# Performance work log

Hardware: AMD Instinct MI355X
Metric: run time of the kernel (lower is better)

## Reference

```python
import jax, jax.numpy as jnp
import numpy as np

NEG = -1e10  # matches the -10000000000.0 boundary padding in the torch code


def nw_forward(theta, A):
    """Needleman-Wunsch forward DP with softmax (logsumexp) operator.

    theta: (B, N, M) match potentials; A: (B,) gap penalty.
    Returns Vt: (B,) terminal alignment scores.
    Recursion: V[i,j] = theta[i-1,j-1] + logsumexp(A+V[i-1,j], V[i-1,j-1], A+V[i,j-1]).
    Implemented as scan over rows (i) with an inner scan over columns (j),
    which honors the sequential DP dependencies without Python loops.
    """
    B, N, M = theta.shape
    dtype = theta.dtype
    # V[0, :] row: V[0,0]=0, V[0,j]=NEG for j>=1
    row0 = jnp.full((B, M + 1), NEG, dtype).at[:, 0].set(0.0)

    def row_step(prev_row, th_row):
        # prev_row: (B, M+1) = V[i-1, 0..M]; th_row: (B, M) = theta[:, i-1, :]
        v_up = prev_row[:, 1:]     # V[i-1, j],   j = 1..M
        v_diag = prev_row[:, :-1]  # V[i-1, j-1], j = 1..M

        def col_step(v_left, inp):
            th_j, vu, vd = inp  # each (B,)
            # order (x, m, y) = (A+up, diag, A+left), matching torch stack(v1,v2,v3)
            v = jnp.stack([A + vu, vd, A + v_left], axis=-1)  # (B, 3)
            v_new = th_j + jax.nn.logsumexp(v, axis=-1)
            return v_new, v_new

        xs = (th_row.T, v_up.T, v_diag.T)  # leading axis M
        v_init = jnp.full((B,), NEG, dtype)  # V[i, 0]
        _, row_vals = jax.lax.scan(col_step, v_init, xs)  # (M, B)
        new_row = jnp.concatenate(
            [jnp.full((B, 1), NEG, dtype), row_vals.T], axis=1)  # (B, M+1)
        return new_row, None

    last_row, _ = jax.lax.scan(row_step, row0, jnp.moveaxis(theta, 1, 0))
    return last_row[:, M]  # Vt = V[:, N, M]


def setup_inputs() -> dict:
    key = jax.random.key(0)
    k1, k2 = jax.random.split(key)
    B, N, M = 32, 512, 512
    theta = jax.random.normal(k1, (B, N, M), dtype=jnp.float32)
    A = jax.random.normal(k2, (B,), dtype=jnp.float32)
    return {"theta": theta, "A": A}


def reference(theta, A):
    return nw_forward(theta, A)
```

## Files before the change

kernel.cpp:

```cpp
#include <hip/hip_runtime.h>
#include <math.h>

#define NEGV  -10000000000.0f
#define LOG2E 1.44269504088896340736f
#define LN2F  0.69314718055994530942f

typedef float f4 __attribute__((ext_vector_type(4)));

constexpr int CS    = 32;
constexpr int ROWS  = 96;
constexpr int WL    = 33;
constexpr int CHW   = ROWS * WL;
constexpr int KCMAX = 32;
constexpr int SIT   = 48;

__global__ __launch_bounds__(512, 2) void nw_kernel(
    const float* __restrict__ theta, const float* __restrict__ A,
    float* __restrict__ out, int N, int M)
{
    __shared__ float thS[8 * CHW];
    __shared__ float bndD[9 * KCMAX * CS];
    __shared__ int   flg[9 * KCMAX];

    const int tid = threadIdx.x;
    const int w   = tid >> 6;
    const int l   = tid & 63;
    const int j   = tid;
    const int b   = blockIdx.x;
    const int NW  = blockDim.x >> 6;

    for (int i = tid; i < 9 * KCMAX; i += blockDim.x) flg[i] = 0;
    __syncthreads();

    const float a2 = A[b] * LOG2E;
    const float* __restrict__ thb = theta + (size_t)b * N * M;
    const int NM = N * M;

    const int T  = N + M - 1;
    const int KC = (T + CS - 1) / CS;
    const int wstart = 64 * w;
    const int wend   = 64 * w + 63 + N - 1;
    const int ca = wstart / CS;
    const int cb = min(KC - 1, wend / CS);

    const int srow = l >> 5;
    const int sq   = l & 31;
    const int lanebase = srow * (M - 1) + 64 * w + 63 + sq;
    const int wrbase   = w * CHW + srow * WL + sq;
    const int rdbase   = w * CHW + (63 - l) * WL;

    auto stage_load = [&](int cn, float* stg) {
        const int rb = CS * cn - 64 * w - 63;
        if (rb >= 0 && rb + (ROWS - 1) <= N - 1) {
            const float* p = thb + (size_t)rb * M;
            #pragma unroll
            for (int it = 0; it < SIT; ++it) { stg[it] = p[lanebase]; p += 2 * (M - 1); }
        } else {
            const int rbM = rb * M;
            #pragma unroll
            for (int it = 0; it < SIT; ++it) {
                int off = rbM + lanebase + it * 2 * (M - 1);
                off = min(max(off, 0), NM - 1);
                stg[it] = thb[off];
            }
        }
    };
    auto stage_write = [&](const float* stg) {
        #pragma unroll
        for (int it = 0; it < SIT; ++it) thS[wrbase + it * 2 * WL] = stg[it] * LOG2E;
    };
    auto wait_flag = [&](int idx) {
        if (__atomic_load_n(&flg[idx], __ATOMIC_ACQUIRE) == 0) {
            do { __builtin_amdgcn_s_sleep(1); }
            while (__atomic_load_n(&flg[idx], __ATOMIC_ACQUIRE) == 0);
        }
    };

    float mp = NEGV, sp = 1.0f;
    float md = (j == 0) ? 0.0f : NEGV, sd = 1.0f;
    float bcarry = NEGV;

    {
        float s0[SIT];
        stage_load(ca, s0);
        stage_write(s0);
        __asm__ volatile("s_waitcnt lgkmcnt(0)" ::: "memory");
    }
    if (w > 0) {
        wait_flag(w * KCMAX + (ca - 1));
        bcarry = bndD[(w * KCMAX + ca - 1) * CS + (CS - 1)];
    }

    float stg[SIT];
    bool have = (ca + 1 <= cb);
    if (have) stage_load(ca + 1, stg);

    for (int c = ca; c <= cb; ++c) {
        float th[CS];
        #pragma unroll
        for (int k = 0; k < 8; ++k) th[k] = thS[rdbase + k * (WL + 1)];

        const bool need_bv = (w > 0) && (CS * c <= 64 * w + N - 1);
        float bv[CS];
        if (need_bv) {
            wait_flag(w * KCMAX + c);
            const f4* src = (const f4*)&bndD[(w * KCMAX + c) * CS];
            #pragma unroll
            for (int q = 0; q < CS / 4; ++q) {
                f4 t = src[q];
                bv[4*q+0] = t.x; bv[4*q+1] = t.y; bv[4*q+2] = t.z; bv[4*q+3] = t.w;
            }
        } else {
            #pragma unroll
            for (int k = 0; k < CS; ++k) bv[k] = NEGV;
        }

        #pragma unroll
        for (int k = 8; k < CS; ++k) th[k] = thS[rdbase + k * (WL + 1)];

        float res[CS];
        const bool full = (CS * c >= 64 * w + 63) &&
                          (CS * c + CS - 1 <= 64 * w + N - 1);
        if (full) {
            #pragma unroll
            for (int k = 0; k < CS; ++k) {
                float bm = (k == 0) ? bcarry : bv[k - 1];
                float ml = __int_as_float(__builtin_amdgcn_update_dpp(
                    __float_as_int(bm), __float_as_int(mp),
                    0x138 , 0xF, 0xF, false));
                float sl = __int_as_float(__builtin_amdgcn_update_dpp(
                    0x3f800000 , __float_as_int(sp),
                    0x138, 0xF, 0xF, false));
                float u  = a2 + mp;
                float ul = a2 + ml;
                float mx = fmaxf(fmaxf(u, md), ul);
                float e1 = __builtin_amdgcn_exp2f(u  - mx);
                float e2 = __builtin_amdgcn_exp2f(md - mx);
                float e3 = __builtin_amdgcn_exp2f(ul - mx);
                float sn = fmaf(sl, e3, fmaf(sd, e2, sp * e1));
                float mn = th[k] + mx;
                res[k] = mn + __builtin_amdgcn_logf(sn);
                md = ml; sd = sl;
                mp = mn; sp = sn;
            }
        } else {
            const int tmj = CS * c - j;
            #pragma unroll
            for (int k = 0; k < CS; ++k) {
                float bm = (k == 0) ? bcarry : bv[k - 1];
                float ml = __int_as_float(__builtin_amdgcn_update_dpp(
                    __float_as_int(bm), __float_as_int(mp),
                    0x138, 0xF, 0xF, false));
                float sl = __int_as_float(__builtin_amdgcn_update_dpp(
                    0x3f800000, __float_as_int(sp),
                    0x138, 0xF, 0xF, false));
                float u  = a2 + mp;
                float ul = a2 + ml;
                float mx = fmaxf(fmaxf(u, md), ul);
                float e1 = __builtin_amdgcn_exp2f(u  - mx);
                float e2 = __builtin_amdgcn_exp2f(md - mx);
                float e3 = __builtin_amdgcn_exp2f(ul - mx);
                float sn = fmaf(sl, e3, fmaf(sd, e2, sp * e1));
                float mn = th[k] + mx;
                int dt = tmj + k;
                bool act = (unsigned)dt < (unsigned)N;
                float mq = act ? mn : (dt < 0 ? NEGV : mp);
                float sq2 = act ? sn : (dt < 0 ? 1.0f : sp);
                res[k] = mq + __builtin_amdgcn_logf(sq2);
                md = ml; sd = sl;
                mp = mq; sp = sq2;
            }
        }

        if (w < NW - 1 && l == 63) {
            f4* dst = (f4*)&bndD[((w + 1) * KCMAX + c) * CS];
            #pragma unroll
            for (int q = 0; q < CS / 4; ++q)
                dst[q] = (f4){res[4*q+0], res[4*q+1], res[4*q+2], res[4*q+3]};
            __atomic_store_n(&flg[(w + 1) * KCMAX + c], 1, __ATOMIC_RELEASE);
        }
        bcarry = bv[CS - 1];

        {
            int bs = __float_as_int(sp);
            int ex = ((bs >> 23) & 0xff) - 127;
            sp = __int_as_float(bs - (ex << 23));
            mp += (float)ex;
            int bd = __float_as_int(sd);
            int ed = ((bd >> 23) & 0xff) - 127;
            sd = __int_as_float(bd - (ed << 23));
            md += (float)ed;
        }

        if (have) stage_write(stg);
        have = (c + 2 <= cb);
        if (have) stage_load(c + 2, stg);
        __asm__ volatile("s_waitcnt lgkmcnt(0)" ::: "memory");
    }

    if (j == M - 1)
        out[b] = (mp + __builtin_amdgcn_logf(sp)) * LN2F;
}

extern "C" void kernel_launch(void* const* d_in, const int* in_sizes, int n_in,
                              void* d_out, int out_size, void* d_ws, size_t ws_size,
                              hipStream_t stream) {
    const float* theta = (const float*)d_in[0];
    const float* A     = (const float*)d_in[1];
    float* out = (float*)d_out;

    const int B  = in_sizes[1];
    const int NM = in_sizes[0] / B;
    int N = 1;
    while (N * N < NM) N <<= 1;
    const int M = NM / N;

    hipLaunchKernelGGL(nw_kernel, dim3(B), dim3(M), 0, stream,
                       theta, A, out, N, M);
}
```

Before: 178.7 us.

## Stream theta tiles directly to LDS with global_load_lds and swizzled layout

Replaces the register-staged global load plus LDS write (48 registers per thread) with direct global-to-LDS loads. A XOR-style rotation swizzle replaces the padded row layout to avoid bank conflicts. The LOG2E scaling moves into an fma in the recurrence, and prefetch depth drops from two stages ahead to one stage issued during compute. This cuts register pressure and VALU/LDS-store work, but single-buffered LDS reuse requires waiting on lgkmcnt before issuing the next stage and vmcnt at loop end, which may expose load latency.

Result: slower. 256.6 us (+43.6%).

```diff
diff --git a/kernel.cpp b/kernel.cpp
--- a/kernel.cpp
+++ b/kernel.cpp
@@ -9,8 +9,7 @@
 
 constexpr int CS    = 32;
 constexpr int ROWS  = 96;
-constexpr int WL    = 33;
-constexpr int CHW   = ROWS * WL;
+constexpr int CHW   = ROWS * 32;
 constexpr int KCMAX = 32;
 constexpr int SIT   = 48;
 
@@ -43,31 +42,38 @@
     const int ca = wstart / CS;
     const int cb = min(KC - 1, wend / CS);
 
-    const int srow = l >> 5;
-    const int sq   = l & 31;
-    const int lanebase = srow * (M - 1) + 64 * w + 63 + sq;
-    const int wrbase   = w * CHW + srow * WL + sq;
-    const int rdbase   = w * CHW + (63 - l) * WL;
-
-    auto stage_load = [&](int cn, float* stg) {
+    const int l5  = l >> 5, l31 = l & 31;
+    const int q2  = l31 - l5;
+    const int q   = 63 - l;
+    float* thW = &thS[w * CHW];
+
+    auto issue_stage = [&](int cn) {
         const int rb = CS * cn - 64 * w - 63;
+        const int gbase = rb * M + 64 * w + 63;
         if (rb >= 0 && rb + (ROWS - 1) <= N - 1) {
-            const float* p = thb + (size_t)rb * M;
-            #pragma unroll
-            for (int it = 0; it < SIT; ++it) { stg[it] = p[lanebase]; p += 2 * (M - 1); }
+            #pragma unroll
+            for (int it = 0; it < SIT; ++it) {
+                const int r = 2 * it + l5;
+                const int c = (q2 - 2 * it) & 31;
+                const int gidx = gbase + r * (M - 1) + c;
+                __builtin_amdgcn_global_load_lds(
+                    (const __attribute__((address_space(1))) void*)(thb + gidx),
+                    (__attribute__((address_space(3))) void*)(thW + it * 64),
+                    4, 0, 0);
+            }
         } else {
-            const int rbM = rb * M;
             #pragma unroll
             for (int it = 0; it < SIT; ++it) {
-                int off = rbM + lanebase + it * 2 * (M - 1);
-                off = min(max(off, 0), NM - 1);
-                stg[it] = thb[off];
-            }
-        }
-    };
-    auto stage_write = [&](const float* stg) {
-        #pragma unroll
-        for (int it = 0; it < SIT; ++it) thS[wrbase + it * 2 * WL] = stg[it] * LOG2E;
+                const int r = 2 * it + l5;
+                const int c = (q2 - 2 * it) & 31;
+                int gidx = gbase + r * (M - 1) + c;
+                gidx = min(max(gidx, 0), NM - 1);
+                __builtin_amdgcn_global_load_lds(
+                    (const __attribute__((address_space(1))) void*)(thb + gidx),
+                    (__attribute__((address_space(3))) void*)(thW + it * 64),
+                    4, 0, 0);
+            }
+        }
     };
     auto wait_flag = [&](int idx) {
         if (__atomic_load_n(&flg[idx], __ATOMIC_ACQUIRE) == 0) {
@@ -80,25 +86,18 @@
     float md = (j == 0) ? 0.0f : NEGV, sd = 1.0f;
     float bcarry = NEGV;
 
-    {
-        float s0[SIT];
-        stage_load(ca, s0);
-        stage_write(s0);
-        __asm__ volatile("s_waitcnt lgkmcnt(0)" ::: "memory");
-    }
+    issue_stage(ca);
+    __asm__ volatile("s_waitcnt vmcnt(0)" ::: "memory");
     if (w > 0) {
         wait_flag(w * KCMAX + (ca - 1));
         bcarry = bndD[(w * KCMAX + ca - 1) * CS + (CS - 1)];
     }
 
-    float stg[SIT];
-    bool have = (ca + 1 <= cb);
-    if (have) stage_load(ca + 1, stg);
-
     for (int c = ca; c <= cb; ++c) {
         float th[CS];
         #pragma unroll
-        for (int k = 0; k < 8; ++k) th[k] = thS[rdbase + k * (WL + 1)];
+        for (int k = 0; k < 8; ++k)
+            th[k] = thW[32 * (q + k) + ((2 * k + q) & 31)];
 
         const bool need_bv = (w > 0) && (CS * c <= 64 * w + N - 1);
         float bv[CS];
@@ -106,9 +105,10 @@
             wait_flag(w * KCMAX + c);
             const f4* src = (const f4*)&bndD[(w * KCMAX + c) * CS];
             #pragma unroll
-            for (int q = 0; q < CS / 4; ++q) {
-                f4 t = src[q];
-                bv[4*q+0] = t.x; bv[4*q+1] = t.y; bv[4*q+2] = t.z; bv[4*q+3] = t.w;
+            for (int qd = 0; qd < CS / 4; ++qd) {
+                f4 t = src[qd];
+                bv[4*qd+0] = t.x; bv[4*qd+1] = t.y;
+                bv[4*qd+2] = t.z; bv[4*qd+3] = t.w;
             }
         } else {
             #pragma unroll
@@ -116,7 +116,11 @@
         }
 
         #pragma unroll
-        for (int k = 8; k < CS; ++k) th[k] = thS[rdbase + k * (WL + 1)];
+        for (int k = 8; k < CS; ++k)
+            th[k] = thW[32 * (q + k) + ((2 * k + q) & 31)];
+
+        __asm__ volatile("s_waitcnt lgkmcnt(0)" ::: "memory");
+        if (c + 1 <= cb) issue_stage(c + 1);
 
         float res[CS];
         const bool full = (CS * c >= 64 * w + 63) &&
@@ -138,7 +142,7 @@
                 float e2 = __builtin_amdgcn_exp2f(md - mx);
                 float e3 = __builtin_amdgcn_exp2f(ul - mx);
                 float sn = fmaf(sl, e3, fmaf(sd, e2, sp * e1));
-                float mn = th[k] + mx;
+                float mn = fmaf(th[k], LOG2E, mx);
                 res[k] = mn + __builtin_amdgcn_logf(sn);
                 md = ml; sd = sl;
                 mp = mn; sp = sn;
@@ -161,7 +165,7 @@
                 float e2 = __builtin_amdgcn_exp2f(md - mx);
                 float e3 = __builtin_amdgcn_exp2f(ul - mx);
                 float sn = fmaf(sl, e3, fmaf(sd, e2, sp * e1));
-                float mn = th[k] + mx;
+                float mn = fmaf(th[k], LOG2E, mx);
                 int dt = tmj + k;
                 bool act = (unsigned)dt < (unsigned)N;
                 float mq = act ? mn : (dt < 0 ? NEGV : mp);
@@ -175,8 +179,8 @@
         if (w < NW - 1 && l == 63) {
             f4* dst = (f4*)&bndD[((w + 1) * KCMAX + c) * CS];
             #pragma unroll
-            for (int q = 0; q < CS / 4; ++q)
-                dst[q] = (f4){res[4*q+0], res[4*q+1], res[4*q+2], res[4*q+3]};
+            for (int qd = 0; qd < CS / 4; ++qd)
+                dst[qd] = (f4){res[4*qd+0], res[4*qd+1], res[4*qd+2], res[4*qd+3]};
             __atomic_store_n(&flg[(w + 1) * KCMAX + c], 1, __ATOMIC_RELEASE);
         }
         bcarry = bv[CS - 1];
@@ -192,10 +196,7 @@
             md += (float)ed;
         }
 
-        if (have) stage_write(stg);
-        have = (c + 2 <= cb);
-        if (have) stage_load(c + 2, stg);
-        __asm__ volatile("s_waitcnt lgkmcnt(0)" ::: "memory");
+        __asm__ volatile("s_waitcnt vmcnt(0)" ::: "memory");
     }
 
     if (j == M - 1)
```
